# Optimization experiments

Measured on AMD Instinct MI355X. Metric: run time of the kernel, lower is better.

The kernel has to match this reference:

```python
import jax, jax.numpy as jnp
import numpy as np
import math

HEAD_DIM = 128
LAMBDA_INIT = 0.8
GN_EPS = 1e-05
NEG = -1e9


def ghostmax(scores):
    # softmax with an extra implicit zero logit (softmax-plus-one)
    m = jnp.maximum(jnp.max(scores, axis=-1, keepdims=True), 0.0)
    e = jnp.exp(scores - m)
    return e / (jnp.sum(e, axis=-1, keepdims=True) + jnp.exp(-m))


def setup_inputs() -> dict:
    key = jax.random.key(0)
    ks = jax.random.split(key, 8)
    B, H2, H, S, D = 2, 16, 8, 2048, HEAD_DIM
    return {
        "q": jax.random.normal(ks[0], (B, H2, S, D), dtype=jnp.float32),
        "k": jax.random.normal(ks[1], (B, H2, S, D), dtype=jnp.float32),
        "v": jax.random.normal(ks[2], (B, H, S, D), dtype=jnp.float32),
        "lambda_q1": 0.1 * jax.random.normal(ks[3], (D,), dtype=jnp.float32),
        "lambda_k1": 0.1 * jax.random.normal(ks[4], (D,), dtype=jnp.float32),
        "lambda_q2": 0.1 * jax.random.normal(ks[5], (D,), dtype=jnp.float32),
        "lambda_k2": 0.1 * jax.random.normal(ks[6], (D,), dtype=jnp.float32),
        "gn_weight": jnp.ones((H * D,), dtype=jnp.float32),
        "gn_bias": jnp.zeros((H * D,), dtype=jnp.float32),
    }


def reference(q, k, v, lambda_q1, lambda_k1, lambda_q2, lambda_k2, gn_weight, gn_bias):
    B, H2, S, D = q.shape
    H = H2 // 2
    scaling = 1.0 / math.sqrt(D)
    # [B, 2H, S, S] attention scores
    scores = jnp.einsum("bhsd,bhtd->bhst", q, k) * scaling
    causal_mask = jnp.triu(jnp.full((S, S), NEG, dtype=scores.dtype), k=1)
    scores = scores + causal_mask[None, None]
    w = ghostmax(scores)
    w = w.reshape(B, H, 2, S, S)
    lam = (
        jnp.exp(jnp.sum(lambda_q1 * lambda_k1))
        - jnp.exp(jnp.sum(lambda_q2 * lambda_k2))
        + LAMBDA_INIT
    )
    w = w[:, :, 0] - lam * w[:, :, 1]  # [B, H, S, S]
    out = jnp.einsum("bhst,bhtd->bhsd", w, v)  # [B, H, S, D]
    # torch .reshape(B, -1, S): raw row-major reinterpretation
    out = out.reshape(B, H * D, S)
    # GroupNorm: num_groups=H over channels H*D, normalized over (group channels, seq)
    g = out.reshape(B, H, D * S)
    mean = jnp.mean(g, axis=-1, keepdims=True)
    var = jnp.var(g, axis=-1, keepdims=True)
    g = (g - mean) * jax.lax.rsqrt(var + GN_EPS)
    out = g.reshape(B, H * D, S) * gn_weight[None, :, None] + gn_bias[None, :, None]
    return out * (1.0 - LAMBDA_INIT)
```

## Files before the change

### kernel.cpp

```cpp
#include <hip/hip_runtime.h>
#include <hip/hip_bf16.h>
#include <cstddef>
#include <cstdint>


typedef __bf16 bf16x8 __attribute__((ext_vector_type(8)));
typedef __bf16 bf16x4 __attribute__((ext_vector_type(4)));
typedef float f32x4 __attribute__((ext_vector_type(4)));

constexpr int SEQ = 2048;
constexpr int DH  = 128;
constexpr int NH  = 8;
constexpr int NH2 = 16;
constexpr float SCALE  = 0.088388347648318447f;
constexpr float QSCALE = 0.127517430f;

template <bool B> struct BoolK { static constexpr bool value = B; };

constexpr size_t QK_ELEMS = (size_t)2 * NH2 * SEQ * DH;
constexpr size_t V_ELEMS  = (size_t)2 * NH  * SEQ * DH;
constexpr size_t OFF_KB   = 4096;
constexpr size_t OFF_VT   = OFF_KB + QK_ELEMS * 2;
constexpr size_t WS_NEED  = OFF_VT + V_ELEMS * 2;

__device__ __forceinline__ void load_lds16(const void* g, void* l) {
  __builtin_amdgcn_global_load_lds(
      (const __attribute__((address_space(1))) uint32_t*)g,
      (__attribute__((address_space(3))) uint32_t*)l, 16, 0, 0);
}

__device__ __forceinline__ bf16x8 cvt8(float4 a, float4 b) {
  bf16x8 r;
  r[0] = (__bf16)a.x; r[1] = (__bf16)a.y; r[2] = (__bf16)a.z; r[3] = (__bf16)a.w;
  r[4] = (__bf16)b.x; r[5] = (__bf16)b.y; r[6] = (__bf16)b.z; r[7] = (__bf16)b.w;
  return r;
}

__global__ __launch_bounds__(256) void prep_kernel(
    const float* __restrict__ k, const float* __restrict__ v,
    __bf16* __restrict__ Kb, __bf16* __restrict__ Vtb,
    float* __restrict__ stats)
{
  __shared__ float tile[32][33];
  const int id = blockIdx.x;
  if (id == 0 && threadIdx.x < 64) stats[threadIdx.x] = 0.f;
  if (id < 4096) {
    const size_t i = ((size_t)id * 256 + threadIdx.x) * 8;
    float4 a = *(const float4*)(k + i);
    float4 b = *(const float4*)(k + i + 4);
    *(bf16x8*)(Kb + i) = cvt8(a, b);
  } else {
    const int vid = id - 4096;
    const int tt = vid & 63, dt = (vid >> 6) & 3, bh = vid >> 8;
    const int tr = threadIdx.x >> 3, tc = (threadIdx.x & 7) * 4;
    const float* src = v + ((size_t)bh * SEQ + tt * 32) * DH + dt * 32;
    float4 f = *(const float4*)(src + (size_t)tr * DH + tc);
    tile[tr][tc + 0] = f.x; tile[tr][tc + 1] = f.y;
    tile[tr][tc + 2] = f.z; tile[tr][tc + 3] = f.w;
    __syncthreads();
    __bf16* dst = Vtb + ((size_t)bh * DH + dt * 32 + tr) * SEQ + tt * 32 + tc;
    bf16x4 o;
    o[0] = (__bf16)tile[tc + 0][tr];
    o[1] = (__bf16)tile[tc + 1][tr];
    o[2] = (__bf16)tile[tc + 2][tr];
    o[3] = (__bf16)tile[tc + 3][tr];
    *(bf16x4*)dst = o;
  }
}

__global__ __launch_bounds__(512, 4) void attn3_kernel(
    const float* __restrict__ Qf, const __bf16* __restrict__ Kb,
    const __bf16* __restrict__ Vtb,
    const float* __restrict__ lq1, const float* __restrict__ lk1,
    const float* __restrict__ lq2, const float* __restrict__ lk2,
    float* __restrict__ Obuf, float* __restrict__ stats)
{
  __shared__ __align__(16) __bf16 ldsK[2][2][32][128];
  __shared__ __align__(16) __bf16 ldsVt[2][128][32];
  __shared__ __align__(16) __bf16 ldsP[2][4][16][36];

  const int bid = (int)blockIdx.x;
  int qt, bh;
  if (bid < 256) { qt = 31 - (bid >> 4); bh = bid & 15; }
  else           { qt = (bid - 256) >> 4; bh = bid & 15; }
  const int b = bh >> 3, h = bh & 7;
  const int tid = threadIdx.x;
  const int g  = tid >> 8;
  const int t2 = tid & 255;
  const int w  = t2 >> 6;
  const int ws = tid >> 6;
  const int lane = tid & 63;
  const int l15 = lane & 15, quad = lane >> 4;

  float a1 = lq1[lane]*lk1[lane] + lq1[lane+64]*lk1[lane+64];
  float a2 = lq2[lane]*lk2[lane] + lq2[lane+64]*lk2[lane+64];
  #pragma unroll
  for (int off = 1; off < 64; off <<= 1) {
    a1 += __shfl_xor(a1, off);
    a2 += __shfl_xor(a2, off);
  }
  const float lam = __expf(a1) - __expf(a2) + 0.8f;

  const size_t headQK = (size_t)(b*NH2 + 2*h + g) * SEQ * DH;
  const float*  Qh  = Qf + headQK;
  const __bf16* Kh  = Kb + headQK;
  const __bf16* Vth = Vtb + (size_t)(b*NH + h) * DH * SEQ;

  size_t goffK[2];
  #pragma unroll
  for (int i = 0; i < 2; ++i) {
    const int R  = w*8 + i*4 + quad;
    const int cs = lane & 15;
    goffK[i] = (size_t)R * DH + ((cs ^ (R & 15)) * 8);
  }
  const int vd = ws*16 + (lane >> 2);
  const size_t goffV = (size_t)vd * SEQ + (((lane & 3) ^ (vd & 3)) * 8);

  __bf16* ldsKg = &ldsK[g][0][0][0];
  __bf16* ldsVb = &ldsVt[0][0][0];

  const int qb = qt * 64;
  const int nsteps = 2*qt + 2;

  const int qrow = qb + w*16 + l15;
  bf16x8 qf[4];
  {
    const float* src = Qh + (size_t)qrow*DH + quad*8;
    #pragma unroll
    for (int kd = 0; kd < 4; ++kd) {
      float4 f0 = *(const float4*)(src + kd*32);
      float4 f1 = *(const float4*)(src + kd*32 + 4);
      f0.x *= QSCALE; f0.y *= QSCALE; f0.z *= QSCALE; f0.w *= QSCALE;
      f1.x *= QSCALE; f1.y *= QSCALE; f1.z *= QSCALE; f1.w *= QSCALE;
      qf[kd] = cvt8(f0, f1);
    }
  }

  f32x4 oacc[8];
  float lsum[4];
  #pragma unroll
  for (int nt = 0; nt < 8; ++nt) oacc[nt] = (f32x4){0.f,0.f,0.f,0.f};
  #pragma unroll
  for (int r = 0; r < 4; ++r) lsum[r] = 0.f;

  {
    #pragma unroll
    for (int i = 0; i < 2; ++i)
      load_lds16(Kh + goffK[i], ldsKg + w*1024 + i*512);
    load_lds16(Vth + goffV, ldsVb + ws*512);
  }
  __syncthreads();

  for (int st = 0; st < nsteps; ++st) {
    const int cur = st & 1;
    const int kbt = st * 32;

    if (st + 1 < nsteps) {
      const int nxt = cur ^ 1;
      const __bf16* kg = Kh + (size_t)(kbt + 32) * DH;
      #pragma unroll
      for (int i = 0; i < 2; ++i)
        load_lds16(kg + goffK[i], ldsKg + nxt*4096 + w*1024 + i*512);
      load_lds16(Vth + (kbt + 32) + goffV, ldsVb + nxt*4096 + ws*512);
    }

    f32x4 sacc[2];
    sacc[0] = (f32x4){0.f,0.f,0.f,0.f};
    sacc[1] = (f32x4){0.f,0.f,0.f,0.f};
    __builtin_amdgcn_s_setprio(1);
    #pragma unroll
    for (int n = 0; n < 2; ++n)
      #pragma unroll
      for (int kd = 0; kd < 4; ++kd) {
        bf16x8 kf = *(const bf16x8*)&ldsK[g][cur][n*16 + l15][((kd*4 + quad) ^ l15) * 8];
        sacc[n] = __builtin_amdgcn_mfma_f32_16x16x32_bf16(qf[kd], kf, sacc[n], 0, 0, 0);
      }
    __builtin_amdgcn_s_setprio(0);

    const int qrow0 = qb + w*16 + quad*4;
    auto sm_body = [&](auto MASKC) {
      constexpr bool MASKED = decltype(MASKC)::value;
      #pragma unroll
      for (int r = 0; r < 4; ++r) {
        float p0 = __builtin_amdgcn_exp2f(sacc[0][r]);
        float p1 = __builtin_amdgcn_exp2f(sacc[1][r]);
        if constexpr (MASKED) {
          const int qr = qrow0 + r;
          if (kbt + l15      > qr) p0 = 0.f;
          if (kbt + l15 + 16 > qr) p1 = 0.f;
        }
        lsum[r] += p0 + p1;
        ldsP[g][w][quad*4 + r][l15]      = (__bf16)p0;
        ldsP[g][w][quad*4 + r][l15 + 16] = (__bf16)p1;
      }
    };
    if (kbt + 31 <= qb + w*16) sm_body(BoolK<false>{});
    else                       sm_body(BoolK<true>{});

    {
      bf16x8 pf = *(const bf16x8*)&ldsP[g][w][l15][quad*8];
      __builtin_amdgcn_s_setprio(1);
      #pragma unroll
      for (int nt = 0; nt < 8; ++nt) {
        bf16x8 vf = *(const bf16x8*)&ldsVt[cur][nt*16 + l15][(quad ^ (l15 & 3)) * 8];
        oacc[nt] = __builtin_amdgcn_mfma_f32_16x16x32_bf16(pf, vf, oacc[nt], 0, 0, 0);
      }
      __builtin_amdgcn_s_setprio(0);
    }
    __syncthreads();
  }

  float lr[4];
  #pragma unroll
  for (int r = 0; r < 4; ++r) {
    float vsum = lsum[r];
    #pragma unroll
    for (int off = 1; off < 16; off <<= 1) vsum += __shfl_xor(vsum, off);
    lr[r] = vsum;
  }

  float* Oscr  = (float*)&ldsK[0][0][0][0];
  float* ldsLa = (float*)&ldsP[0][0][0][0];
  if (g == 1) {
    #pragma unroll
    for (int nt = 0; nt < 8; ++nt)
      #pragma unroll
      for (int r = 0; r < 4; ++r)
        Oscr[(w*16 + quad*4 + r)*128 + nt*16 + l15] = oacc[nt][r];
    if (l15 == 0) {
      #pragma unroll
      for (int r = 0; r < 4; ++r)
        ldsLa[w*16 + quad*4 + r] = lr[r];
    }
  }
  __syncthreads();

  if (g == 0) {
    const int qrow0 = qb + w*16 + quad*4;
    float* obase = Obuf + (size_t)(b*NH + h) * SEQ * DH;
    float sum = 0.f, ss = 0.f;
    #pragma unroll
    for (int r = 0; r < 4; ++r) {
      const float l0 = lr[r] + 1.0f;
      const float l1 = ldsLa[w*16 + quad*4 + r] + 1.0f;
      const float i0 = 1.0f / l0;
      const float i1 = lam / l1;
      float* orow = obase + (size_t)(qrow0 + r) * DH + l15;
      #pragma unroll
      for (int nt = 0; nt < 8; ++nt) {
        const float o1 = Oscr[(w*16 + quad*4 + r)*128 + nt*16 + l15];
        const float val = oacc[nt][r] * i0 - o1 * i1;
        orow[nt*16] = val;
        sum += val;
        ss  += val * val;
      }
    }
    #pragma unroll
    for (int off = 1; off < 64; off <<= 1) {
      sum += __shfl_xor(sum, off);
      ss  += __shfl_xor(ss, off);
    }
    if (lane == 0) {
      atomicAdd(&stats[2*(b*NH + h)],     sum);
      atomicAdd(&stats[2*(b*NH + h) + 1], ss);
    }
  }
}

__global__ __launch_bounds__(256) void attn_fb_kernel(
    const float* __restrict__ q, const float* __restrict__ k,
    const float* __restrict__ v,
    const float* __restrict__ lq1, const float* __restrict__ lk1,
    const float* __restrict__ lq2, const float* __restrict__ lk2,
    float* __restrict__ Obuf, float* __restrict__ stats)
{
  __shared__ __align__(16) __bf16 lds_k[2][32][136];
  __shared__ __align__(16) __bf16 lds_vt[128][40];
  __shared__ __align__(16) __bf16 lds_p[4][2][16][40];

  const int qt = blockIdx.x, h = blockIdx.y, b = blockIdx.z;
  const int qb = qt * 64;
  const int tid = threadIdx.x;
  const int w = tid >> 6, lane = tid & 63;
  const int l15 = lane & 15, quad = lane >> 4;

  float a1 = lq1[lane]*lk1[lane] + lq1[lane+64]*lk1[lane+64];
  float a2 = lq2[lane]*lk2[lane] + lq2[lane+64]*lk2[lane+64];
  #pragma unroll
  for (int off = 1; off < 64; off <<= 1) {
    a1 += __shfl_xor(a1, off);
    a2 += __shfl_xor(a2, off);
  }
  const float lam = __expf(a1) - __expf(a2) + 0.8f;

  const float* qh0 = q + (size_t)(b*NH2 + 2*h) * SEQ * DH;
  const float* qh1 = qh0 + (size_t)SEQ * DH;
  const float* kh0 = k + (size_t)(b*NH2 + 2*h) * SEQ * DH;
  const float* kh1 = kh0 + (size_t)SEQ * DH;
  const float* vh  = v + (size_t)(b*NH + h) * SEQ * DH;

  bf16x8 qf[2][4];
  {
    const int qrow = qb + w*16 + l15;
    #pragma unroll
    for (int sh = 0; sh < 2; ++sh) {
      const float* src = (sh ? qh1 : qh0) + (size_t)qrow * DH + quad*8;
      #pragma unroll
      for (int kd = 0; kd < 4; ++kd) {
        float4 f0 = *(const float4*)(src + kd*32);
        float4 f1 = *(const float4*)(src + kd*32 + 4);
        qf[sh][kd] = cvt8(f0, f1);
      }
    }
  }

  f32x4 oacc[2][8];
  #pragma unroll
  for (int sh = 0; sh < 2; ++sh)
    #pragma unroll
    for (int nt = 0; nt < 8; ++nt)
      oacc[sh][nt] = (f32x4){0.f,0.f,0.f,0.f};

  float mst[2][4] = {{0.f,0.f,0.f,0.f},{0.f,0.f,0.f,0.f}};
  float lst[2][4] = {{1.f,1.f,1.f,1.f},{1.f,1.f,1.f,1.f}};

  const int krow = tid >> 2, ksh = krow >> 5, kr = krow & 31;
  const int kd0 = (tid & 3) * 32;
  const float* ksrc0 = (ksh ? kh1 : kh0) + kd0;
  const int vt = tid >> 3, vd = (tid & 7) * 16;

  const int nsteps = (qb + 64) / 32;
  for (int st = 0; st < nsteps; ++st) {
    const int kbt = st * 32;
    {
      const float* sp = ksrc0 + (size_t)(kbt + kr) * DH;
      #pragma unroll
      for (int c = 0; c < 4; ++c) {
        float4 f0 = *(const float4*)(sp + c*8);
        float4 f1 = *(const float4*)(sp + c*8 + 4);
        *(bf16x8*)&lds_k[ksh][kr][kd0 + c*8] = cvt8(f0, f1);
      }
      const float* vp = vh + (size_t)(kbt + vt) * DH + vd;
      #pragma unroll
      for (int c = 0; c < 4; ++c) {
        float4 f = *(const float4*)(vp + c*4);
        lds_vt[vd + c*4 + 0][vt] = (__bf16)f.x;
        lds_vt[vd + c*4 + 1][vt] = (__bf16)f.y;
        lds_vt[vd + c*4 + 2][vt] = (__bf16)f.z;
        lds_vt[vd + c*4 + 3][vt] = (__bf16)f.w;
      }
    }
    __syncthreads();

    f32x4 sacc[2][2];
    #pragma unroll
    for (int sh = 0; sh < 2; ++sh)
      #pragma unroll
      for (int n = 0; n < 2; ++n)
        sacc[sh][n] = (f32x4){0.f,0.f,0.f,0.f};

    #pragma unroll
    for (int sh = 0; sh < 2; ++sh)
      #pragma unroll
      for (int n = 0; n < 2; ++n)
        #pragma unroll
        for (int kd = 0; kd < 4; ++kd) {
          bf16x8 bf = *(const bf16x8*)&lds_k[sh][n*16 + l15][kd*32 + quad*8];
          sacc[sh][n] = __builtin_amdgcn_mfma_f32_16x16x32_bf16(qf[sh][kd], bf, sacc[sh][n], 0, 0, 0);
        }

    const int qrow0 = qb + w*16 + quad*4;
    const int c0 = kbt + l15, c1 = c0 + 16;
    #pragma unroll
    for (int sh = 0; sh < 2; ++sh) {
      #pragma unroll
      for (int r = 0; r < 4; ++r) {
        float s0 = sacc[sh][0][r] * SCALE;
        float s1 = sacc[sh][1][r] * SCALE;
        const int qr = qrow0 + r;
        if (c0 > qr) s0 = -1e30f;
        if (c1 > qr) s1 = -1e30f;
        float mx = fmaxf(s0, s1);
        #pragma unroll
        for (int off = 1; off < 16; off <<= 1)
          mx = fmaxf(mx, __shfl_xor(mx, off));
        const float mnew = fmaxf(mst[sh][r], mx);
        const float alpha = __expf(mst[sh][r] - mnew);
        mst[sh][r] = mnew;
        const float p0 = __expf(s0 - mnew);
        const float p1 = __expf(s1 - mnew);
        float rs = p0 + p1;
        #pragma unroll
        for (int off = 1; off < 16; off <<= 1)
          rs += __shfl_xor(rs, off);
        lst[sh][r] = lst[sh][r] * alpha + rs;
        #pragma unroll
        for (int nt = 0; nt < 8; ++nt)
          oacc[sh][nt][r] *= alpha;
        lds_p[w][sh][quad*4 + r][l15]      = (__bf16)p0;
        lds_p[w][sh][quad*4 + r][l15 + 16] = (__bf16)p1;
      }
    }

    {
      bf16x8 pf0 = *(const bf16x8*)&lds_p[w][0][l15][quad*8];
      bf16x8 pf1 = *(const bf16x8*)&lds_p[w][1][l15][quad*8];
      #pragma unroll
      for (int nt = 0; nt < 8; ++nt) {
        bf16x8 vf = *(const bf16x8*)&lds_vt[nt*16 + l15][quad*8];
        oacc[0][nt] = __builtin_amdgcn_mfma_f32_16x16x32_bf16(pf0, vf, oacc[0][nt], 0, 0, 0);
        oacc[1][nt] = __builtin_amdgcn_mfma_f32_16x16x32_bf16(pf1, vf, oacc[1][nt], 0, 0, 0);
      }
    }
    __syncthreads();
  }

  const int qrow0 = qb + w*16 + quad*4;
  float* obase = Obuf + (size_t)(b*NH + h) * SEQ * DH;
  float sum = 0.f, ss = 0.f;
  #pragma unroll
  for (int r = 0; r < 4; ++r) {
    const float i0 = 1.0f / lst[0][r];
    const float i1 = lam / lst[1][r];
    float* orow = obase + (size_t)(qrow0 + r) * DH + l15;
    #pragma unroll
    for (int nt = 0; nt < 8; ++nt) {
      const float val = oacc[0][nt][r] * i0 - oacc[1][nt][r] * i1;
      orow[nt*16] = val;
      sum += val;
      ss  += val * val;
    }
  }
  #pragma unroll
  for (int off = 1; off < 64; off <<= 1) {
    sum += __shfl_xor(sum, off);
    ss  += __shfl_xor(ss, off);
  }
  if (lane == 0) {
    atomicAdd(&stats[2*(b*NH + h)],     sum);
    atomicAdd(&stats[2*(b*NH + h) + 1], ss);
  }
}

__global__ __launch_bounds__(256) void norm_kernel(
    float* __restrict__ Obuf, const float* __restrict__ stats,
    const float* __restrict__ gw, const float* __restrict__ gb)
{
  const int idx = (blockIdx.x * 256 + threadIdx.x) * 4;
  const int bh = idx >> 18;
  const int local = idx & 262143;
  const float inv = 1.0f / 262144.0f;
  const float mean = stats[2*bh] * inv;
  const float var  = stats[2*bh + 1] * inv - mean * mean;
  const float rstd = rsqrtf(var + 1e-5f);
  const int c = ((bh & 7) << 7) + (local >> 11);
  const float wq = gw[c] * rstd;
  const float bq = gb[c];
  float4 o = *(const float4*)(Obuf + idx);
  float4 r;
  r.x = ((o.x - mean) * wq + bq) * 0.2f;
  r.y = ((o.y - mean) * wq + bq) * 0.2f;
  r.z = ((o.z - mean) * wq + bq) * 0.2f;
  r.w = ((o.w - mean) * wq + bq) * 0.2f;
  *(float4*)(Obuf + idx) = r;
}

extern "C" void kernel_launch(void* const* d_in, const int* in_sizes, int n_in,
                              void* d_out, int out_size, void* d_ws, size_t ws_size,
                              hipStream_t stream) {
  const float* q   = (const float*)d_in[0];
  const float* k   = (const float*)d_in[1];
  const float* v   = (const float*)d_in[2];
  const float* lq1 = (const float*)d_in[3];
  const float* lk1 = (const float*)d_in[4];
  const float* lq2 = (const float*)d_in[5];
  const float* lk2 = (const float*)d_in[6];
  const float* gw  = (const float*)d_in[7];
  const float* gb  = (const float*)d_in[8];
  float* out = (float*)d_out;
  float* stats = (float*)d_ws;

  if (ws_size >= WS_NEED) {
    __bf16* Kb  = (__bf16*)((char*)d_ws + OFF_KB);
    __bf16* Vtb = (__bf16*)((char*)d_ws + OFF_VT);

    prep_kernel<<<8192, 256, 0, stream>>>(k, v, Kb, Vtb, stats);

    attn3_kernel<<<512, 512, 0, stream>>>(q, Kb, Vtb,
        lq1, lk1, lq2, lk2, out, stats);
  } else {
    (void)hipMemsetAsync(d_ws, 0, 256, stream);
    attn_fb_kernel<<<dim3(32, NH, 2), 256, 0, stream>>>(q, k, v,
        lq1, lk1, lq2, lk2, out, stats);
  }

  const int total = 2 * NH * SEQ * DH;
  norm_kernel<<<total / 1024, 256, 0, stream>>>(out, stats, gw, gb);
}
```

Before: 203.5 us.

## Give each wave two 16-row query tiles and halve block thread count

```diff
diff --git a/kernel.cpp b/kernel.cpp
--- a/kernel.cpp
+++ b/kernel.cpp
@@ -68,7 +68,7 @@
   }
 }
 
-__global__ __launch_bounds__(512, 4) void attn3_kernel(
+__global__ __launch_bounds__(256, 2) void attn3_kernel(
     const float* __restrict__ Qf, const __bf16* __restrict__ Kb,
     const __bf16* __restrict__ Vtb,
     const float* __restrict__ lq1, const float* __restrict__ lk1,
@@ -77,7 +77,8 @@
 {
   __shared__ __align__(16) __bf16 ldsK[2][2][32][128];
   __shared__ __align__(16) __bf16 ldsVt[2][128][32];
-  __shared__ __align__(16) __bf16 ldsP[2][4][16][36];
+  __shared__ __align__(16) __bf16 ldsP[4][32][36];
+  __shared__ float ldsLa[64];
 
   const int bid = (int)blockIdx.x;
   int qt, bh;
@@ -85,10 +86,9 @@
   else           { qt = (bid - 256) >> 4; bh = bid & 15; }
   const int b = bh >> 3, h = bh & 7;
   const int tid = threadIdx.x;
-  const int g  = tid >> 8;
-  const int t2 = tid & 255;
-  const int w  = t2 >> 6;
-  const int ws = tid >> 6;
+  const int wv = tid >> 6;
+  const int g  = wv >> 1;
+  const int w2 = wv & 1;
   const int lane = tid & 63;
   const int l15 = lane & 15, quad = lane >> 4;
 
@@ -106,48 +106,59 @@
   const __bf16* Kh  = Kb + headQK;
   const __bf16* Vth = Vtb + (size_t)(b*NH + h) * DH * SEQ;
 
-  size_t goffK[2];
+  size_t goffK[4];
+  #pragma unroll
+  for (int i = 0; i < 4; ++i) {
+    const int c  = i*128 + w2*64 + lane;
+    const int R  = c >> 4, cs = c & 15;
+    goffK[i] = (size_t)R * DH + ((cs ^ (R & 15)) * 8);
+  }
+  size_t goffV[2];
   #pragma unroll
   for (int i = 0; i < 2; ++i) {
-    const int R  = w*8 + i*4 + quad;
-    const int cs = lane & 15;
-    goffK[i] = (size_t)R * DH + ((cs ^ (R & 15)) * 8);
-  }
-  const int vd = ws*16 + (lane >> 2);
-  const size_t goffV = (size_t)vd * SEQ + (((lane & 3) ^ (vd & 3)) * 8);
+    const int c  = i*256 + tid;
+    const int d  = c >> 2, cs = c & 3;
+    goffV[i] = (size_t)d * SEQ + ((cs ^ (d & 3)) * 8);
+  }
 
   __bf16* ldsKg = &ldsK[g][0][0][0];
   __bf16* ldsVb = &ldsVt[0][0][0];
 
   const int qb = qt * 64;
   const int nsteps = 2*qt + 2;
-
-  const int qrow = qb + w*16 + l15;
-  bf16x8 qf[4];
-  {
-    const float* src = Qh + (size_t)qrow*DH + quad*8;
+  const int rbase = qb + w2*32;
+
+  bf16x8 qf[2][4];
+  #pragma unroll
+  for (int mi = 0; mi < 2; ++mi) {
+    const float* src = Qh + (size_t)(rbase + mi*16 + l15)*DH + quad*8;
     #pragma unroll
     for (int kd = 0; kd < 4; ++kd) {
       float4 f0 = *(const float4*)(src + kd*32);
       float4 f1 = *(const float4*)(src + kd*32 + 4);
       f0.x *= QSCALE; f0.y *= QSCALE; f0.z *= QSCALE; f0.w *= QSCALE;
       f1.x *= QSCALE; f1.y *= QSCALE; f1.z *= QSCALE; f1.w *= QSCALE;
-      qf[kd] = cvt8(f0, f1);
-    }
-  }
-
-  f32x4 oacc[8];
-  float lsum[4];
-  #pragma unroll
-  for (int nt = 0; nt < 8; ++nt) oacc[nt] = (f32x4){0.f,0.f,0.f,0.f};
-  #pragma unroll
-  for (int r = 0; r < 4; ++r) lsum[r] = 0.f;
+      qf[mi][kd] = cvt8(f0, f1);
+    }
+  }
+
+  f32x4 oacc[2][8];
+  float lsum[2][4];
+  #pragma unroll
+  for (int mi = 0; mi < 2; ++mi) {
+    #pragma unroll
+    for (int nt = 0; nt < 8; ++nt) oacc[mi][nt] = (f32x4){0.f,0.f,0.f,0.f};
+    #pragma unroll
+    for (int r = 0; r < 4; ++r) lsum[mi][r] = 0.f;
+  }
 
   {
     #pragma unroll
+    for (int i = 0; i < 4; ++i)
+      load_lds16(Kh + goffK[i], ldsKg + i*1024 + w2*512);
+    #pragma unroll
     for (int i = 0; i < 2; ++i)
-      load_lds16(Kh + goffK[i], ldsKg + w*1024 + i*512);
-    load_lds16(Vth + goffV, ldsVb + ws*512);
+      load_lds16(Vth + goffV[i], ldsVb + i*2048 + wv*512);
   }
   __syncthreads();
 
@@ -159,102 +170,117 @@
       const int nxt = cur ^ 1;
       const __bf16* kg = Kh + (size_t)(kbt + 32) * DH;
       #pragma unroll
+      for (int i = 0; i < 4; ++i)
+        load_lds16(kg + goffK[i], ldsKg + nxt*4096 + i*1024 + w2*512);
+      #pragma unroll
       for (int i = 0; i < 2; ++i)
-        load_lds16(kg + goffK[i], ldsKg + nxt*4096 + w*1024 + i*512);
-      load_lds16(Vth + (kbt + 32) + goffV, ldsVb + nxt*4096 + ws*512);
-    }
-
-    f32x4 sacc[2];
-    sacc[0] = (f32x4){0.f,0.f,0.f,0.f};
-    sacc[1] = (f32x4){0.f,0.f,0.f,0.f};
+        load_lds16(Vth + (kbt + 32) + goffV[i], ldsVb + nxt*4096 + i*2048 + wv*512);
+    }
+
+    f32x4 sacc[2][2];
+    #pragma unroll
+    for (int mi = 0; mi < 2; ++mi) {
+      sacc[mi][0] = (f32x4){0.f,0.f,0.f,0.f};
+      sacc[mi][1] = (f32x4){0.f,0.f,0.f,0.f};
+    }
     __builtin_amdgcn_s_setprio(1);
     #pragma unroll
     for (int n = 0; n < 2; ++n)
       #pragma unroll
       for (int kd = 0; kd < 4; ++kd) {
         bf16x8 kf = *(const bf16x8*)&ldsK[g][cur][n*16 + l15][((kd*4 + quad) ^ l15) * 8];
-        sacc[n] = __builtin_amdgcn_mfma_f32_16x16x32_bf16(qf[kd], kf, sacc[n], 0, 0, 0);
+        sacc[0][n] = __builtin_amdgcn_mfma_f32_16x16x32_bf16(qf[0][kd], kf, sacc[0][n], 0, 0, 0);
+        sacc[1][n] = __builtin_amdgcn_mfma_f32_16x16x32_bf16(qf[1][kd], kf, sacc[1][n], 0, 0, 0);
       }
     __builtin_amdgcn_s_setprio(0);
 
-    const int qrow0 = qb + w*16 + quad*4;
     auto sm_body = [&](auto MASKC) {
       constexpr bool MASKED = decltype(MASKC)::value;
       #pragma unroll
-      for (int r = 0; r < 4; ++r) {
-        float p0 = __builtin_amdgcn_exp2f(sacc[0][r]);
-        float p1 = __builtin_amdgcn_exp2f(sacc[1][r]);
-        if constexpr (MASKED) {
-          const int qr = qrow0 + r;
-          if (kbt + l15      > qr) p0 = 0.f;
-          if (kbt + l15 + 16 > qr) p1 = 0.f;
+      for (int mi = 0; mi < 2; ++mi)
+        #pragma unroll
+        for (int r = 0; r < 4; ++r) {
+          float p0 = __builtin_amdgcn_exp2f(sacc[mi][0][r]);
+          float p1 = __builtin_amdgcn_exp2f(sacc[mi][1][r]);
+          if constexpr (MASKED) {
+            const int qr = rbase + mi*16 + quad*4 + r;
+            if (kbt + l15      > qr) p0 = 0.f;
+            if (kbt + l15 + 16 > qr) p1 = 0.f;
+          }
+          lsum[mi][r] += p0 + p1;
+          ldsP[wv][mi*16 + quad*4 + r][l15]      = (__bf16)p0;
+          ldsP[wv][mi*16 + quad*4 + r][l15 + 16] = (__bf16)p1;
         }
-        lsum[r] += p0 + p1;
-        ldsP[g][w][quad*4 + r][l15]      = (__bf16)p0;
-        ldsP[g][w][quad*4 + r][l15 + 16] = (__bf16)p1;
-      }
     };
-    if (kbt + 31 <= qb + w*16) sm_body(BoolK<false>{});
-    else                       sm_body(BoolK<true>{});
+    if (kbt + 31 <= rbase) sm_body(BoolK<false>{});
+    else                   sm_body(BoolK<true>{});
 
     {
-      bf16x8 pf = *(const bf16x8*)&ldsP[g][w][l15][quad*8];
+      bf16x8 pf0 = *(const bf16x8*)&ldsP[wv][l15][quad*8];
+      bf16x8 pf1 = *(const bf16x8*)&ldsP[wv][16 + l15][quad*8];
       __builtin_amdgcn_s_setprio(1);
       #pragma unroll
       for (int nt = 0; nt < 8; ++nt) {
         bf16x8 vf = *(const bf16x8*)&ldsVt[cur][nt*16 + l15][(quad ^ (l15 & 3)) * 8];
-        oacc[nt] = __builtin_amdgcn_mfma_f32_16x16x32_bf16(pf, vf, oacc[nt], 0, 0, 0);
+        oacc[0][nt] = __builtin_amdgcn_mfma_f32_16x16x32_bf16(pf0, vf, oacc[0][nt], 0, 0, 0);
+        oacc[1][nt] = __builtin_amdgcn_mfma_f32_16x16x32_bf16(pf1, vf, oacc[1][nt], 0, 0, 0);
       }
       __builtin_amdgcn_s_setprio(0);
     }
     __syncthreads();
   }
 
-  float lr[4];
-  #pragma unroll
-  for (int r = 0; r < 4; ++r) {
-    float vsum = lsum[r];
-    #pragma unroll
-    for (int off = 1; off < 16; off <<= 1) vsum += __shfl_xor(vsum, off);
-    lr[r] = vsum;
-  }
-
-  float* Oscr  = (float*)&ldsK[0][0][0][0];
-  float* ldsLa = (float*)&ldsP[0][0][0][0];
+  float lr[2][4];
+  #pragma unroll
+  for (int mi = 0; mi < 2; ++mi)
+    #pragma unroll
+    for (int r = 0; r < 4; ++r) {
+      float vsum = lsum[mi][r];
+      #pragma unroll
+      for (int off = 1; off < 16; off <<= 1) vsum += __shfl_xor(vsum, off);
+      lr[mi][r] = vsum;
+    }
+
+  float* Oscr = (float*)&ldsK[0][0][0][0];
   if (g == 1) {
     #pragma unroll
-    for (int nt = 0; nt < 8; ++nt)
-      #pragma unroll
-      for (int r = 0; r < 4; ++r)
-        Oscr[(w*16 + quad*4 + r)*128 + nt*16 + l15] = oacc[nt][r];
-    if (l15 == 0) {
-      #pragma unroll
-      for (int r = 0; r < 4; ++r)
-        ldsLa[w*16 + quad*4 + r] = lr[r];
+    for (int mi = 0; mi < 2; ++mi) {
+      #pragma unroll
+      for (int nt = 0; nt < 8; ++nt)
+        #pragma unroll
+        for (int r = 0; r < 4; ++r)
+          Oscr[(w2*32 + mi*16 + quad*4 + r)*128 + nt*16 + l15] = oacc[mi][nt][r];
+      if (l15 == 0) {
+        #pragma unroll
+        for (int r = 0; r < 4; ++r)
+          ldsLa[w2*32 + mi*16 + quad*4 + r] = lr[mi][r];
+      }
     }
   }
   __syncthreads();
 
   if (g == 0) {
-    const int qrow0 = qb + w*16 + quad*4;
     float* obase = Obuf + (size_t)(b*NH + h) * SEQ * DH;
     float sum = 0.f, ss = 0.f;
     #pragma unroll
-    for (int r = 0; r < 4; ++r) {
-      const float l0 = lr[r] + 1.0f;
-      const float l1 = ldsLa[w*16 + quad*4 + r] + 1.0f;
-      const float i0 = 1.0f / l0;
-      const float i1 = lam / l1;
-      float* orow = obase + (size_t)(qrow0 + r) * DH + l15;
-      #pragma unroll
-      for (int nt = 0; nt < 8; ++nt) {
-        const float o1 = Oscr[(w*16 + quad*4 + r)*128 + nt*16 + l15];
-        const float val = oacc[nt][r] * i0 - o1 * i1;
-        orow[nt*16] = val;
-        sum += val;
-        ss  += val * val;
-      }
-    }
+    for (int mi = 0; mi < 2; ++mi)
+      #pragma unroll
+      for (int r = 0; r < 4; ++r) {
+        const int row = w2*32 + mi*16 + quad*4 + r;
+        const float l0 = lr[mi][r] + 1.0f;
+        const float l1 = ldsLa[row] + 1.0f;
+        const float i0 = 1.0f / l0;
+        const float i1 = lam / l1;
+        float* orow = obase + (size_t)(qb + row) * DH + l15;
+        #pragma unroll
+        for (int nt = 0; nt < 8; ++nt) {
+          const float o1 = Oscr[row*128 + nt*16 + l15];
+          const float val = oacc[mi][nt][r] * i0 - o1 * i1;
+          orow[nt*16] = val;
+          sum += val;
+          ss  += val * val;
+        }
+      }
     #pragma unroll
     for (int off = 1; off < 64; off <<= 1) {
       sum += __shfl_xor(sum, off);
@@ -486,7 +512,7 @@
 
     prep_kernel<<<8192, 256, 0, stream>>>(k, v, Kb, Vtb, stats);
 
-    attn3_kernel<<<512, 512, 0, stream>>>(q, Kb, Vtb,
+    attn3_kernel<<<512, 256, 0, stream>>>(q, Kb, Vtb,
         lq1, lk1, lq2, lk2, out, stats);
   } else {
     (void)hipMemsetAsync(d_ws, 0, 256, stream);
```

After: 212.7 us. 4.5% more time.

## Halve attention query tile to 32 rows with 256-thread blocks

Applied to the files above, without the earlier changes.

```diff
diff --git a/kernel.cpp b/kernel.cpp
--- a/kernel.cpp
+++ b/kernel.cpp
@@ -68,7 +68,7 @@
   }
 }
 
-__global__ __launch_bounds__(512, 4) void attn3_kernel(
+__global__ __launch_bounds__(256, 3) void attn3_kernel(
     const float* __restrict__ Qf, const __bf16* __restrict__ Kb,
     const __bf16* __restrict__ Vtb,
     const float* __restrict__ lq1, const float* __restrict__ lk1,
@@ -77,18 +77,17 @@
 {
   __shared__ __align__(16) __bf16 ldsK[2][2][32][128];
   __shared__ __align__(16) __bf16 ldsVt[2][128][32];
-  __shared__ __align__(16) __bf16 ldsP[2][4][16][36];
+  __shared__ __align__(16) __bf16 ldsP[4][16][36];
+  __shared__ float ldsLa[32];
 
   const int bid = (int)blockIdx.x;
-  int qt, bh;
-  if (bid < 256) { qt = 31 - (bid >> 4); bh = bid & 15; }
-  else           { qt = (bid - 256) >> 4; bh = bid & 15; }
+  const int qt = 63 - (bid >> 4);
+  const int bh = bid & 15;
   const int b = bh >> 3, h = bh & 7;
   const int tid = threadIdx.x;
-  const int g  = tid >> 8;
-  const int t2 = tid & 255;
-  const int w  = t2 >> 6;
-  const int ws = tid >> 6;
+  const int wv = tid >> 6;
+  const int g  = wv >> 1;
+  const int w2 = wv & 1;
   const int lane = tid & 63;
   const int l15 = lane & 15, quad = lane >> 4;
 
@@ -106,26 +105,31 @@
   const __bf16* Kh  = Kb + headQK;
   const __bf16* Vth = Vtb + (size_t)(b*NH + h) * DH * SEQ;
 
-  size_t goffK[2];
+  size_t goffK[4];
+  #pragma unroll
+  for (int i = 0; i < 4; ++i) {
+    const int c  = i*128 + w2*64 + lane;
+    const int R  = c >> 4, cs = c & 15;
+    goffK[i] = (size_t)R * DH + ((cs ^ (R & 15)) * 8);
+  }
+  size_t goffV[2];
   #pragma unroll
   for (int i = 0; i < 2; ++i) {
-    const int R  = w*8 + i*4 + quad;
-    const int cs = lane & 15;
-    goffK[i] = (size_t)R * DH + ((cs ^ (R & 15)) * 8);
-  }
-  const int vd = ws*16 + (lane >> 2);
-  const size_t goffV = (size_t)vd * SEQ + (((lane & 3) ^ (vd & 3)) * 8);
+    const int c  = i*256 + tid;
+    const int d  = c >> 2, cs = c & 3;
+    goffV[i] = (size_t)d * SEQ + ((cs ^ (d & 3)) * 8);
+  }
 
   __bf16* ldsKg = &ldsK[g][0][0][0];
   __bf16* ldsVb = &ldsVt[0][0][0];
 
-  const int qb = qt * 64;
-  const int nsteps = 2*qt + 2;
-
-  const int qrow = qb + w*16 + l15;
+  const int qb = qt * 32;
+  const int nsteps = qt + 1;
+  const int rbase = qb + w2*16;
+
   bf16x8 qf[4];
   {
-    const float* src = Qh + (size_t)qrow*DH + quad*8;
+    const float* src = Qh + (size_t)(rbase + l15)*DH + quad*8;
     #pragma unroll
     for (int kd = 0; kd < 4; ++kd) {
       float4 f0 = *(const float4*)(src + kd*32);
@@ -145,9 +149,11 @@
 
   {
     #pragma unroll
+    for (int i = 0; i < 4; ++i)
+      load_lds16(Kh + goffK[i], ldsKg + i*1024 + w2*512);
+    #pragma unroll
     for (int i = 0; i < 2; ++i)
-      load_lds16(Kh + goffK[i], ldsKg + w*1024 + i*512);
-    load_lds16(Vth + goffV, ldsVb + ws*512);
+      load_lds16(Vth + goffV[i], ldsVb + i*2048 + wv*512);
   }
   __syncthreads();
 
@@ -159,9 +165,11 @@
       const int nxt = cur ^ 1;
       const __bf16* kg = Kh + (size_t)(kbt + 32) * DH;
       #pragma unroll
+      for (int i = 0; i < 4; ++i)
+        load_lds16(kg + goffK[i], ldsKg + nxt*4096 + i*1024 + w2*512);
+      #pragma unroll
       for (int i = 0; i < 2; ++i)
-        load_lds16(kg + goffK[i], ldsKg + nxt*4096 + w*1024 + i*512);
-      load_lds16(Vth + (kbt + 32) + goffV, ldsVb + nxt*4096 + ws*512);
+        load_lds16(Vth + (kbt + 32) + goffV[i], ldsVb + nxt*4096 + i*2048 + wv*512);
     }
 
     f32x4 sacc[2];
@@ -177,7 +185,6 @@
       }
     __builtin_amdgcn_s_setprio(0);
 
-    const int qrow0 = qb + w*16 + quad*4;
     auto sm_body = [&](auto MASKC) {
       constexpr bool MASKED = decltype(MASKC)::value;
       #pragma unroll
@@ -185,20 +192,20 @@
         float p0 = __builtin_amdgcn_exp2f(sacc[0][r]);
         float p1 = __builtin_amdgcn_exp2f(sacc[1][r]);
         if constexpr (MASKED) {
-          const int qr = qrow0 + r;
+          const int qr = rbase + quad*4 + r;
           if (kbt + l15      > qr) p0 = 0.f;
           if (kbt + l15 + 16 > qr) p1 = 0.f;
         }
         lsum[r] += p0 + p1;
-        ldsP[g][w][quad*4 + r][l15]      = (__bf16)p0;
-        ldsP[g][w][quad*4 + r][l15 + 16] = (__bf16)p1;
+        ldsP[wv][quad*4 + r][l15]      = (__bf16)p0;
+        ldsP[wv][quad*4 + r][l15 + 16] = (__bf16)p1;
       }
     };
-    if (kbt + 31 <= qb + w*16) sm_body(BoolK<false>{});
-    else                       sm_body(BoolK<true>{});
+    if (kbt + 31 <= rbase) sm_body(BoolK<false>{});
+    else                   sm_body(BoolK<true>{});
 
     {
-      bf16x8 pf = *(const bf16x8*)&ldsP[g][w][l15][quad*8];
+      bf16x8 pf = *(const bf16x8*)&ldsP[wv][l15][quad*8];
       __builtin_amdgcn_s_setprio(1);
       #pragma unroll
       for (int nt = 0; nt < 8; ++nt) {
@@ -219,36 +226,35 @@
     lr[r] = vsum;
   }
 
-  float* Oscr  = (float*)&ldsK[0][0][0][0];
-  float* ldsLa = (float*)&ldsP[0][0][0][0];
+  float* Oscr = (float*)&ldsK[0][0][0][0];
   if (g == 1) {
     #pragma unroll
     for (int nt = 0; nt < 8; ++nt)
       #pragma unroll
       for (int r = 0; r < 4; ++r)
-        Oscr[(w*16 + quad*4 + r)*128 + nt*16 + l15] = oacc[nt][r];
+        Oscr[(w2*16 + quad*4 + r)*128 + nt*16 + l15] = oacc[nt][r];
     if (l15 == 0) {
       #pragma unroll
       for (int r = 0; r < 4; ++r)
-        ldsLa[w*16 + quad*4 + r] = lr[r];
+        ldsLa[w2*16 + quad*4 + r] = lr[r];
     }
   }
   __syncthreads();
 
   if (g == 0) {
-    const int qrow0 = qb + w*16 + quad*4;
     float* obase = Obuf + (size_t)(b*NH + h) * SEQ * DH;
     float sum = 0.f, ss = 0.f;
     #pragma unroll
     for (int r = 0; r < 4; ++r) {
+      const int row = w2*16 + quad*4 + r;
       const float l0 = lr[r] + 1.0f;
-      const float l1 = ldsLa[w*16 + quad*4 + r] + 1.0f;
+      const float l1 = ldsLa[row] + 1.0f;
       const float i0 = 1.0f / l0;
       const float i1 = lam / l1;
-      float* orow = obase + (size_t)(qrow0 + r) * DH + l15;
+      float* orow = obase + (size_t)(qb + row) * DH + l15;
       #pragma unroll
       for (int nt = 0; nt < 8; ++nt) {
-        const float o1 = Oscr[(w*16 + quad*4 + r)*128 + nt*16 + l15];
+        const float o1 = Oscr[row*128 + nt*16 + l15];
         const float val = oacc[nt][r] * i0 - o1 * i1;
         orow[nt*16] = val;
         sum += val;
@@ -486,7 +492,7 @@
 
     prep_kernel<<<8192, 256, 0, stream>>>(k, v, Kb, Vtb, stats);
 
-    attn3_kernel<<<512, 512, 0, stream>>>(q, Kb, Vtb,
+    attn3_kernel<<<1024, 256, 0, stream>>>(q, Kb, Vtb,
         lq1, lk1, lq2, lk2, out, stats);
   } else {
     (void)hipMemsetAsync(d_ws, 0, 256, stream);
```

After: 211.9 us. 4.1% more time.
